# Performance work log

Measured on AMD Instinct MI355X. Metric: run time of the kernel, lower is better.

## Reference

```python
import jax, jax.numpy as jnp
import numpy as np

KS = 5          # kernel_size per pseudo-dim
DIM = 2         # pseudo-coordinate dims
KTOT = KS ** DIM  # 25 spline kernel slots
N_NODES = 50000
N_EDGES = 1600000
N_GRAPHS = 64
F_IN, H1, H2, N_CLS = 32, 32, 64, 10


def spline_basis(edge_attr):
    """Open B-spline basis, degree 1, dim=2, kernel_size=5.
    Returns basis [E,4] and flat kernel indices [E,4]."""
    v = edge_attr * (KS - 1)                    # [E,2] in [0, KS-1]
    lo = jnp.floor(v)
    frac = v - lo                               # [E,2]
    lo_i = lo.astype(jnp.int32)
    # per-dim basis values for offsets s in {0,1}: (1-frac), frac
    bas_d = jnp.stack([1.0 - frac, frac], axis=-1)            # [E,2,2]
    idx_d = jnp.minimum(lo_i[..., None] + jnp.arange(2, dtype=jnp.int32), KS - 1)  # [E,2,2]
    basis = bas_d[:, 0, :, None] * bas_d[:, 1, None, :]       # [E,2,2]
    kidx = idx_d[:, 0, :, None] + KS * idx_d[:, 1, None, :]   # [E,2,2]
    E = edge_attr.shape[0]
    return basis.reshape(E, 4), kidx.reshape(E, 4)


def spline_conv(x, src, dst, basis, kidx, W, Wroot, b):
    """SplineConv: gather x[src], spline-weight, scatter-mean to dst, + root + bias.
    W: [KTOT, Cin, Cout]."""
    N, Cin = x.shape
    x_j = x[src]                                # [E, Cin] gather
    # accumulate per-(node, kernel-slot) weighted sums; loop over 4 nonzero combos
    T = jnp.zeros((N * KTOT, Cin), dtype=x.dtype)
    for s in range(4):
        seg = dst * KTOT + kidx[:, s]
        T = T + jax.ops.segment_sum(basis[:, s, None] * x_j, seg,
                                    num_segments=N * KTOT)
    T = T.reshape(N, KTOT, Cin)
    out = jnp.einsum('nki,kio->no', T, W)       # [N, Cout]
    deg = jax.ops.segment_sum(jnp.ones_like(dst, dtype=x.dtype), dst,
                              num_segments=N)
    out = out / jnp.maximum(deg, 1.0)[:, None]  # aggr='mean'
    return out + x @ Wroot + b


def global_mean_pool(x, batch, num_graphs):
    s = jax.ops.segment_sum(x, batch, num_segments=num_graphs)
    cnt = jax.ops.segment_sum(jnp.ones((x.shape[0],), x.dtype), batch,
                              num_segments=num_graphs)
    return s / jnp.maximum(cnt, 1.0)[:, None]


def setup_inputs() -> dict:
    key = jax.random.key(0)
    ks = jax.random.split(key, 16)
    x = jax.random.normal(ks[0], (N_NODES, F_IN), jnp.float32)
    edge_index = jax.random.randint(ks[1], (2, N_EDGES), 0, N_NODES, jnp.int32)
    edge_attr = jax.random.uniform(ks[2], (N_EDGES, DIM), jnp.float32)
    batch = jnp.sort(jax.random.randint(ks[3], (N_NODES,), 0, N_GRAPHS, jnp.int32))

    def w(k, shape, fan_in):
        return jax.random.normal(k, shape, jnp.float32) / np.sqrt(fan_in)

    return {
        'x': x, 'edge_index': edge_index, 'edge_attr': edge_attr, 'batch': batch,
        'W1': w(ks[4], (KTOT, F_IN, H1), F_IN), 'root1': w(ks[5], (F_IN, H1), F_IN),
        'b1': jnp.zeros((H1,), jnp.float32),
        'W2': w(ks[6], (KTOT, H1, H2), H1), 'root2': w(ks[7], (H1, H2), H1),
        'b2': jnp.zeros((H2,), jnp.float32),
        'lin1_w': w(ks[8], (H2, 64), H2), 'lin1_b': jnp.zeros((64,), jnp.float32),
        'lin2_w': w(ks[9], (64, 64), 64), 'lin2_b': jnp.zeros((64,), jnp.float32),
        'lin3_w': w(ks[10], (64, N_CLS), 64), 'lin3_b': jnp.zeros((N_CLS,), jnp.float32),
    }


def reference(x, edge_index, edge_attr, batch, W1, root1, b1, W2, root2, b2,
              lin1_w, lin1_b, lin2_w, lin2_b, lin3_w, lin3_b):
    src, dst = edge_index[0], edge_index[1]
    basis, kidx = spline_basis(edge_attr)
    h = jax.nn.relu(spline_conv(x, src, dst, basis, kidx, W1, root1, b1))
    h = jax.nn.relu(spline_conv(h, src, dst, basis, kidx, W2, root2, b2))
    g = global_mean_pool(h, batch, N_GRAPHS)                # [B, 64]
    g = g * jax.nn.sigmoid(g @ lin1_w + lin1_b)
    g = g * jax.nn.sigmoid(g @ lin2_w + lin2_b)
    return jax.nn.log_softmax(g @ lin3_w + lin3_b, axis=1)  # [B, N_CLS]
```

## Files before the change

kernel.cpp:

```cpp
#include <hip/hip_runtime.h>
#include <hip/hip_bf16.h>
#include <hip/hip_fp16.h>
#include <cstdint>


typedef _Float16 half8 __attribute__((ext_vector_type(8)));
typedef float f32x4 __attribute__((ext_vector_type(4)));
typedef float f32x2 __attribute__((ext_vector_type(2)));

__device__ __forceinline__ int h2_as_int(__half2 h) {
  int v; __builtin_memcpy(&v, &h, 4); return v;
}
__device__ __forceinline__ __half2 int_as_h2(int v) {
  __half2 h; __builtin_memcpy(&h, &v, 4); return h;
}

__device__ __forceinline__ int lowb(const int* __restrict__ a, int n, int v) {
  int lo = 0, hi = n;
  while (lo < hi) { int m = (lo + hi) >> 1; if (a[m] < v) lo = m + 1; else hi = m; }
  return lo;
}

__global__ void hist_kernel(const int* __restrict__ dst, int E, int* __restrict__ deg) {
  int e = blockIdx.x * 256 + threadIdx.x;
  if (e < E) atomicAdd(&deg[dst[e]], 1);
}

__global__ __launch_bounds__(1024) void scan_block_kernel(
    const int* __restrict__ deg, int n, int* __restrict__ offs, int* __restrict__ bsums) {
  __shared__ int wsum[16];
  int t = threadIdx.x;
  int gi = blockIdx.x * 1024 + t;
  int v = (gi < n) ? deg[gi] : 0;
  int lane = t & 63, w = t >> 6;
  int x = v;
  #pragma unroll
  for (int d = 1; d < 64; d <<= 1) { int y = __shfl_up(x, d, 64); if (lane >= d) x += y; }
  if (lane == 63) wsum[w] = x;
  __syncthreads();
  if (w == 0) {
    int s = (lane < 16) ? wsum[lane] : 0;
    #pragma unroll
    for (int d = 1; d < 16; d <<= 1) { int y = __shfl_up(s, d, 64); if (lane >= d) s += y; }
    if (lane < 16) wsum[lane] = s;
  }
  __syncthreads();
  int add = (w > 0) ? wsum[w - 1] : 0;
  x += add;
  if (gi < n) offs[gi + 1] = x;
  if (t == 1023) bsums[blockIdx.x] = x;
}

__global__ __launch_bounds__(64) void scan_bsums_kernel(
    const int* __restrict__ bsums, int nb, int* __restrict__ boff) {
  int l = threadIdx.x;
  int v = (l < nb) ? bsums[l] : 0;
  int x = v;
  #pragma unroll
  for (int d = 1; d < 64; d <<= 1) { int y = __shfl_up(x, d, 64); if (l >= d) x += y; }
  if (l < nb) boff[l] = x - v;
}

__global__ void scan_add_kernel(int* __restrict__ offs, const int* __restrict__ boff, int n) {
  int i = blockIdx.x * 256 + threadIdx.x;
  if (i < n) offs[i + 1] += boff[i >> 10];
  if (i == 0) offs[0] = 0;
}

__global__ void posinit_kernel(const int* __restrict__ offs, int* __restrict__ pos, int n) {
  int i = blockIdx.x * 256 + threadIdx.x;
  if (i < n) pos[i] = offs[i];
}

__global__ void scatter_kernel(const int* __restrict__ src, const int* __restrict__ dst,
                               const float2* __restrict__ attr, int E,
                               int* __restrict__ pos, int4* __restrict__ emeta) {
  int e = blockIdx.x * 256 + threadIdx.x;
  if (e < E) {
    float2 a = attr[e];
    float v0 = a.x * 4.f, v1 = a.y * 4.f;
    int i00 = min((int)v0, 3);
    int i10 = min((int)v1, 3);
    float f0 = v0 - (float)i00;
    float f1 = v1 - (float)i10;
    float w00 = (1.f - f0) * (1.f - f1);
    float w10 = f0 * (1.f - f1);
    float w01 = (1.f - f0) * f1;
    float w11 = f0 * f1;
    int d = dst[e];
    int p = atomicAdd(&pos[d], 1);
    emeta[p] = make_int4(src[e], i10 * 5 + i00,
                         h2_as_int(__floats2half2_rn(w00, w10)),
                         h2_as_int(__floats2half2_rn(w01, w11)));
  }
}

__global__ void x2h_kernel(const float* __restrict__ X, __half* __restrict__ Xh, int n) {
  int i = blockIdx.x * 256 + threadIdx.x;
  if (i < n) Xh[i] = __float2half(X[i]);
}

__global__ void w2h_kernel(const float* __restrict__ W, __half* __restrict__ Wh,
                           int ncolTot, int COUT) {
  int idx = blockIdx.x * 256 + threadIdx.x;
  if (idx < ncolTot * 32) {
    int col = idx >> 5, i = idx & 31;
    int kk = col / COUT, ch = col - kk * COUT;
    Wh[idx] = __float2half(W[(kk * 32 + i) * COUT + ch]);
  }
}

template <bool FP8>
__global__ __launch_bounds__(256) void mfma_ygemm(
    const __half* __restrict__ Xh, const __half* __restrict__ Wh,
    char* __restrict__ Y, int N, int ncol, int rowBytes) {
  constexpr int EB = FP8 ? 1 : 2;
  constexpr int LSTR = FP8 ? 272 : 528;
  __shared__ __align__(16) char Ls[16 * LSTR];
  const int t = threadIdx.x;
  const int w = t >> 6, lane = t & 63;
  const int rowBase = blockIdx.x * 16;
  const int colBase = blockIdx.y * 256;
  const int kOff = (lane >> 4) * 8;
  int arow = min(rowBase + (lane & 15), N - 1);
  const half8 Af = *(const half8*)(Xh + (size_t)arow * 32 + kOff);
  half8 Bf[4];
  #pragma unroll
  for (int c = 0; c < 4; ++c) {
    int col = min(colBase + w * 64 + c * 16 + (lane & 15), ncol - 1);
    Bf[c] = *(const half8*)(Wh + (size_t)col * 32 + kOff);
  }
  f32x4 zero = {0.f, 0.f, 0.f, 0.f};
  f32x4 acc[4];
  #pragma unroll
  for (int c = 0; c < 4; ++c)
    acc[c] = __builtin_amdgcn_mfma_f32_16x16x32_f16(Af, Bf[c], zero, 0, 0, 0);
  #pragma unroll
  for (int c = 0; c < 4; ++c) {
    int col = w * 64 + c * 16 + (lane & 15);
    int r0 = (lane >> 4) * 4;
    #pragma unroll
    for (int r = 0; r < 4; ++r) {
      if constexpr (FP8) {
        int pk = __builtin_amdgcn_cvt_pk_fp8_f32(acc[c][r], acc[c][r], 0, false);
        Ls[(r0 + r) * LSTR + col] = (char)(pk & 0xff);
      } else {
        *(__half*)(Ls + (r0 + r) * LSTR + col * 2) = __float2half(acc[c][r]);
      }
    }
  }
  __syncthreads();
  int row = rowBase + (t >> 4);
  int cseg = (t & 15) * 16;
  if (row < N && colBase + cseg < ncol) {
    char* dst = Y + (size_t)row * rowBytes + (size_t)(colBase + cseg) * EB;
    const char* s = Ls + (t >> 4) * LSTR + cseg * EB;
    if constexpr (FP8) {
      *(int4*)dst = *(const int4*)s;
    } else {
      ((int4*)dst)[0] = ((const int4*)s)[0];
      ((int4*)dst)[1] = ((const int4*)s)[1];
    }
  }
}

template <int COUT, bool FP8>
__global__ __launch_bounds__(256) void gather_kernel(
    const int4* __restrict__ emeta, const int* __restrict__ offs,
    const char* __restrict__ Ybase, int rowBytes,
    const __half* __restrict__ X, const float* __restrict__ root,
    const float* __restrict__ bias, __half* __restrict__ hout, int N) {
  __shared__ float Rs[32 * COUT];
  const int t = threadIdx.x;
  #pragma unroll
  for (int q = 0; q < (8 * COUT) / 256; ++q)
    *(float4*)&Rs[(t + q * 256) * 4] = *(const float4*)&root[(t + q * 256) * 4];
  __syncthreads();
  const int w = t >> 6, lane = t & 63;
  const int n = blockIdx.x * 4 + w;
  if (n >= N) return;
  const int q4 = lane >> 4, r = lane & 15;
  const int di0 = q4 & 1, di1 = q4 >> 1;
  constexpr int CPL = COUT / 16;
  constexpr int EB = FP8 ? 1 : 2;
  const int laneByte = (di1 * 5 * COUT + di0 * COUT + r * CPL) * EB;
  const int shiftSel = di0 * 16;
  float acc[CPL];
  #pragma unroll
  for (int j = 0; j < CPL; ++j) acc[j] = 0.f;
  const int beg = offs[n], end = offs[n + 1];
  for (int b0 = beg; b0 < end; b0 += 64) {
    const int cnt = min(64, end - b0);
    int4 m = emeta[b0 + min(lane, cnt - 1)];
    const int myByte = m.x * rowBytes + m.y * (COUT * EB);
    const int myP0 = m.z, myP1 = m.w;
    for (int j0 = 0; j0 < cnt; j0 += 4) {
      int yw[4]; float wq[4];
      #pragma unroll
      for (int u = 0; u < 4; ++u) {
        int j = j0 + u;
        int jc = (j < cnt) ? j : 0;
        int b  = __builtin_amdgcn_readlane(myByte, jc);
        int p0 = __builtin_amdgcn_readlane(myP0, jc);
        int p1 = __builtin_amdgcn_readlane(myP1, jc);
        int pw = (di1 ? p1 : p0) >> shiftSel;
        unsigned short u16 = (unsigned short)pw;
        __half hw; __builtin_memcpy(&hw, &u16, 2);
        float wv = __half2float(hw);
        wq[u] = (j < cnt) ? wv : 0.f;
        yw[u] = *(const int*)(Ybase + (size_t)(unsigned)(b + laneByte));
      }
      #pragma unroll
      for (int u = 0; u < 4; ++u) {
        if constexpr (FP8) {
          f32x2 fa = __builtin_amdgcn_cvt_pk_f32_fp8(yw[u], false);
          f32x2 fb = __builtin_amdgcn_cvt_pk_f32_fp8(yw[u], true);
          acc[0] = fmaf(wq[u], fa[0], acc[0]);
          acc[1] = fmaf(wq[u], fa[1], acc[1]);
          acc[2] = fmaf(wq[u], fb[0], acc[2]);
          acc[3] = fmaf(wq[u], fb[1], acc[3]);
        } else {
          __half2 yv = int_as_h2(yw[u]);
          acc[0] = fmaf(wq[u], __half2float(__low2half(yv)), acc[0]);
          acc[1] = fmaf(wq[u], __half2float(__high2half(yv)), acc[1]);
        }
      }
    }
  }
  #pragma unroll
  for (int j = 0; j < CPL; ++j) {
    acc[j] += __shfl_xor(acc[j], 16);
    acc[j] += __shfl_xor(acc[j], 32);
  }
  const int laneCh = r * CPL;
  if (lane < 16) {
    float rd = 1.f / (float)max(end - beg, 1);
    float a[CPL];
    #pragma unroll
    for (int j = 0; j < CPL; ++j) a[j] = acc[j] * rd;
    const __half* xr = X + (size_t)n * 32;
    for (int i = 0; i < 32; ++i) {
      float xv = __half2float(xr[i]);
      #pragma unroll
      for (int j = 0; j < CPL; ++j)
        a[j] = fmaf(xv, Rs[i * COUT + laneCh + j], a[j]);
    }
    #pragma unroll
    for (int j = 0; j < CPL; ++j) a[j] = fmaxf(a[j] + bias[laneCh + j], 0.f);
    __half2* op = (__half2*)(hout + (size_t)n * COUT + laneCh);
    #pragma unroll
    for (int p = 0; p < CPL / 2; ++p)
      op[p] = __floats2half2_rn(a[2 * p], a[2 * p + 1]);
  }
}

__global__ __launch_bounds__(256) void pool_kernel(
    const __half* __restrict__ h2, const int* __restrict__ batch, int N,
    float* __restrict__ poolacc) {
  __shared__ float red[4][64];
  int g = blockIdx.x >> 2, part = blockIdx.x & 3;
  int lo = lowb(batch, N, g), hi = lowb(batch, N, g + 1);
  int len = hi - lo;
  int b0 = lo + (int)(((long long)len * part) / 4);
  int b1 = lo + (int)(((long long)len * (part + 1)) / 4);
  int r = threadIdx.x >> 6, o = threadIdx.x & 63;
  float s = 0.f;
  for (int row = b0 + r; row < b1; row += 4)
    s += __half2float(h2[(size_t)row * 64 + o]);
  red[r][o] = s;
  __syncthreads();
  if (r == 0) {
    float v = red[0][o] + red[1][o] + red[2][o] + red[3][o];
    atomicAdd(&poolacc[g * 64 + o], v);
  }
}

__global__ __launch_bounds__(64) void head_kernel(
    const float* __restrict__ poolacc, const int* __restrict__ batch, int N,
    const float* __restrict__ w1, const float* __restrict__ b1,
    const float* __restrict__ w2, const float* __restrict__ b2,
    const float* __restrict__ w3, const float* __restrict__ b3,
    float* __restrict__ out) {
  __shared__ float gb[64];
  __shared__ float lg[10];
  int g = blockIdx.x, o = threadIdx.x;
  int lo = lowb(batch, N, g), hi = lowb(batch, N, g + 1);
  float cnt = fmaxf((float)(hi - lo), 1.f);
  float gv = poolacc[g * 64 + o] / cnt;
  gb[o] = gv;
  __syncthreads();
  float tacc = b1[o];
  for (int i = 0; i < 64; ++i) tacc = fmaf(gb[i], w1[i * 64 + o], tacc);
  gv = gv * (1.f / (1.f + expf(-tacc)));
  __syncthreads(); gb[o] = gv; __syncthreads();
  tacc = b2[o];
  for (int i = 0; i < 64; ++i) tacc = fmaf(gb[i], w2[i * 64 + o], tacc);
  gv = gv * (1.f / (1.f + expf(-tacc)));
  __syncthreads(); gb[o] = gv; __syncthreads();
  if (o < 10) {
    float l = b3[o];
    for (int i = 0; i < 64; ++i) l = fmaf(gb[i], w3[i * 10 + o], l);
    lg[o] = l;
  }
  __syncthreads();
  if (o < 10) {
    float m = lg[0];
    #pragma unroll
    for (int c = 1; c < 10; ++c) m = fmaxf(m, lg[c]);
    float s = 0.f;
    #pragma unroll
    for (int c = 0; c < 10; ++c) s += expf(lg[c] - m);
    out[g * 10 + o] = lg[o] - m - logf(s);
  }
}

extern "C" void kernel_launch(void* const* d_in, const int* in_sizes, int n_in,
                              void* d_out, int out_size, void* d_ws, size_t ws_size,
                              hipStream_t stream) {
  const float* x     = (const float*)d_in[0];
  const int*   ei    = (const int*)d_in[1];
  const float* eattr = (const float*)d_in[2];
  const int*   batch = (const int*)d_in[3];
  const float* W1    = (const float*)d_in[4];
  const float* root1 = (const float*)d_in[5];
  const float* b1    = (const float*)d_in[6];
  const float* W2    = (const float*)d_in[7];
  const float* root2 = (const float*)d_in[8];
  const float* b2    = (const float*)d_in[9];
  const float* l1w   = (const float*)d_in[10];
  const float* l1b   = (const float*)d_in[11];
  const float* l2w   = (const float*)d_in[12];
  const float* l2b   = (const float*)d_in[13];
  const float* l3w   = (const float*)d_in[14];
  const float* l3b   = (const float*)d_in[15];
  float* out = (float*)d_out;

  const int N = in_sizes[0] / 32;
  const int E = in_sizes[1] / 2;
  const int Npad = (N + 63) & ~63;

  char* base = (char*)d_ws;
  size_t off = 0;
  auto walloc = [&](size_t bytes) -> void* {
    off = (off + 255) & ~(size_t)255;
    void* p = base + off;
    off += bytes;
    return p;
  };
  int*    deg     = (int*)walloc((size_t)Npad * 4);
  int*    offs    = (int*)walloc((size_t)(N + 1) * 4);
  int*    pos     = (int*)walloc((size_t)N * 4);
  int*    bsums   = (int*)walloc(64 * 4);
  int*    boff    = (int*)walloc(64 * 4);
  float*  poolacc = (float*)walloc(64 * 64 * 4);
  __half* h1h     = (__half*)walloc((size_t)N * 32 * 2);
  __half* h2h     = (__half*)walloc((size_t)N * 64 * 2);
  __half* Xh      = (__half*)walloc((size_t)N * 32 * 2);
  __half* Wh1     = (__half*)walloc((size_t)800 * 32 * 2);
  __half* Wh2     = (__half*)walloc((size_t)1600 * 32 * 2);
  int4*   emeta   = (int4*)walloc((size_t)E * 16);
  off = (off + 255) & ~(size_t)255;
  size_t avail = (ws_size > off) ? (ws_size - off) : 0;
  if (avail < (size_t)N * 1600) return;
  char* Yb = base + off;

  const int* srcA = ei;
  const int* dstA = ei + E;

  hipMemsetAsync(deg, 0, (size_t)Npad * 4, stream);
  hipMemsetAsync(poolacc, 0, 64 * 64 * 4, stream);

  hist_kernel<<<(E + 255) / 256, 256, 0, stream>>>(dstA, E, deg);
  int nb = (N + 1023) / 1024;
  scan_block_kernel<<<nb, 1024, 0, stream>>>(deg, N, offs, bsums);
  scan_bsums_kernel<<<1, 64, 0, stream>>>(bsums, nb, boff);
  scan_add_kernel<<<(N + 255) / 256, 256, 0, stream>>>(offs, boff, N);
  posinit_kernel<<<(N + 255) / 256, 256, 0, stream>>>(offs, pos, N);
  scatter_kernel<<<(E + 255) / 256, 256, 0, stream>>>(srcA, dstA, (const float2*)eattr,
                                                      E, pos, emeta);
  x2h_kernel<<<((size_t)N * 32 + 255) / 256, 256, 0, stream>>>(x, Xh, N * 32);
  w2h_kernel<<<(800 * 32 + 255) / 256, 256, 0, stream>>>(W1, Wh1, 800, 32);
  w2h_kernel<<<(1600 * 32 + 255) / 256, 256, 0, stream>>>(W2, Wh2, 1600, 64);

  const int rowTiles = (N + 15) / 16;
  const int ggrid = (N + 3) / 4;

  mfma_ygemm<false><<<dim3(rowTiles, (800 + 255) / 256), 256, 0, stream>>>(
      Xh, Wh1, Yb, N, 800, 1600);
  gather_kernel<32, false><<<ggrid, 256, 0, stream>>>(
      emeta, offs, Yb, 1600, Xh, root1, b1, h1h, N);

  mfma_ygemm<true><<<dim3(rowTiles, (1600 + 255) / 256), 256, 0, stream>>>(
      h1h, Wh2, Yb, N, 1600, 1600);
  gather_kernel<64, true><<<ggrid, 256, 0, stream>>>(
      emeta, offs, Yb, 1600, h1h, root2, b2, h2h, N);

  pool_kernel<<<256, 256, 0, stream>>>(h2h, batch, N, poolacc);
  head_kernel<<<64, 64, 0, stream>>>(poolacc, batch, N,
                                     l1w, l1b, l2w, l2b, l3w, l3b, out);
}
```

Baseline: 468.7 us.

## Pack edge metadata into 8 bytes and store layer-1 projections as FP8

Edge metadata shrinks from 16 to 8 bytes by bit-packing the source index (16 bits), the kernel slot and 10-bit quantised spline fractions. The gather kernel rebuilds the four basis weights from these fields. Layer 1 now writes its per-slot projection table Y in FP8, halving Y bytes and gather traffic, with the gather reading 2-byte FP8 pairs. This reduces memory traffic in the bandwidth-bound gathers, but it costs accuracy and assumes source indices fit in 16 bits, which breaks for N=50000 > 65535? (50000 < 65536, so it fits).

```diff
diff --git a/kernel.cpp b/kernel.cpp
--- a/kernel.cpp
+++ b/kernel.cpp
@@ -10,9 +10,6 @@
 
 __device__ __forceinline__ int h2_as_int(__half2 h) {
   int v; __builtin_memcpy(&v, &h, 4); return v;
-}
-__device__ __forceinline__ __half2 int_as_h2(int v) {
-  __half2 h; __builtin_memcpy(&h, &v, 4); return h;
 }
 
 __device__ __forceinline__ int lowb(const int* __restrict__ a, int n, int v) {
@@ -74,7 +71,7 @@
 
 __global__ void scatter_kernel(const int* __restrict__ src, const int* __restrict__ dst,
                                const float2* __restrict__ attr, int E,
-                               int* __restrict__ pos, int4* __restrict__ emeta) {
+                               int* __restrict__ pos, int2* __restrict__ emeta) {
   int e = blockIdx.x * 256 + threadIdx.x;
   if (e < E) {
     float2 a = attr[e];
@@ -83,15 +80,12 @@
     int i10 = min((int)v1, 3);
     float f0 = v0 - (float)i00;
     float f1 = v1 - (float)i10;
-    float w00 = (1.f - f0) * (1.f - f1);
-    float w10 = f0 * (1.f - f1);
-    float w01 = (1.f - f0) * f1;
-    float w11 = f0 * f1;
+    int f0q = (int)(f0 * 1023.f + 0.5f);
+    int f1q = (int)(f1 * 1023.f + 0.5f);
+    int k00 = i10 * 5 + i00;
     int d = dst[e];
     int p = atomicAdd(&pos[d], 1);
-    emeta[p] = make_int4(src[e], i10 * 5 + i00,
-                         h2_as_int(__floats2half2_rn(w00, w10)),
-                         h2_as_int(__floats2half2_rn(w01, w11)));
+    emeta[p] = make_int2(src[e] | (k00 << 16) | (f0q << 21), f1q);
   }
 }
 
@@ -166,7 +160,7 @@
 
 template <int COUT, bool FP8>
 __global__ __launch_bounds__(256) void gather_kernel(
-    const int4* __restrict__ emeta, const int* __restrict__ offs,
+    const int2* __restrict__ emeta, const int* __restrict__ offs,
     const char* __restrict__ Ybase, int rowBytes,
     const __half* __restrict__ X, const float* __restrict__ root,
     const float* __restrict__ bias, __half* __restrict__ hout, int N) {
@@ -191,9 +185,15 @@
   const int beg = offs[n], end = offs[n + 1];
   for (int b0 = beg; b0 < end; b0 += 64) {
     const int cnt = min(64, end - b0);
-    int4 m = emeta[b0 + min(lane, cnt - 1)];
-    const int myByte = m.x * rowBytes + m.y * (COUT * EB);
-    const int myP0 = m.z, myP1 = m.w;
+    int2 m = emeta[b0 + min(lane, cnt - 1)];
+    const int sA = m.x & 0xffff;
+    const int k00 = (m.x >> 16) & 31;
+    const float f0 = (float)((m.x >> 21) & 1023) * (1.f / 1023.f);
+    const float f1 = (float)(m.y & 1023) * (1.f / 1023.f);
+    const int myByte = sA * rowBytes + k00 * (COUT * EB);
+    const int myP0 = h2_as_int(__floats2half2_rn((1.f - f0) * (1.f - f1),
+                                                 f0 * (1.f - f1)));
+    const int myP1 = h2_as_int(__floats2half2_rn((1.f - f0) * f1, f0 * f1));
     for (int j0 = 0; j0 < cnt; j0 += 4) {
       int yw[4]; float wq[4];
       #pragma unroll
@@ -208,19 +208,26 @@
         __half hw; __builtin_memcpy(&hw, &u16, 2);
         float wv = __half2float(hw);
         wq[u] = (j < cnt) ? wv : 0.f;
-        yw[u] = *(const int*)(Ybase + (size_t)(unsigned)(b + laneByte));
+        const char* yp = Ybase + (size_t)(unsigned)(b + laneByte);
+        if constexpr (FP8 && CPL == 2) {
+          yw[u] = *(const unsigned short*)yp;
+        } else {
+          yw[u] = *(const int*)yp;
+        }
       }
       #pragma unroll
       for (int u = 0; u < 4; ++u) {
         if constexpr (FP8) {
           f32x2 fa = __builtin_amdgcn_cvt_pk_f32_fp8(yw[u], false);
-          f32x2 fb = __builtin_amdgcn_cvt_pk_f32_fp8(yw[u], true);
           acc[0] = fmaf(wq[u], fa[0], acc[0]);
           acc[1] = fmaf(wq[u], fa[1], acc[1]);
-          acc[2] = fmaf(wq[u], fb[0], acc[2]);
-          acc[3] = fmaf(wq[u], fb[1], acc[3]);
+          if constexpr (CPL == 4) {
+            f32x2 fb = __builtin_amdgcn_cvt_pk_f32_fp8(yw[u], true);
+            acc[2] = fmaf(wq[u], fb[0], acc[2]);
+            acc[3] = fmaf(wq[u], fb[1], acc[3]);
+          }
         } else {
-          __half2 yv = int_as_h2(yw[u]);
+          __half2 yv; __builtin_memcpy(&yv, &yw[u], 4);
           acc[0] = fmaf(wq[u], __half2float(__low2half(yv)), acc[0]);
           acc[1] = fmaf(wq[u], __half2float(__high2half(yv)), acc[1]);
         }
@@ -358,7 +365,7 @@
   __half* Xh      = (__half*)walloc((size_t)N * 32 * 2);
   __half* Wh1     = (__half*)walloc((size_t)800 * 32 * 2);
   __half* Wh2     = (__half*)walloc((size_t)1600 * 32 * 2);
-  int4*   emeta   = (int4*)walloc((size_t)E * 16);
+  int2*   emeta   = (int2*)walloc((size_t)E * 8);
   off = (off + 255) & ~(size_t)255;
   size_t avail = (ws_size > off) ? (ws_size - off) : 0;
   if (avail < (size_t)N * 1600) return;
@@ -385,10 +392,10 @@
   const int rowTiles = (N + 15) / 16;
   const int ggrid = (N + 3) / 4;
 
-  mfma_ygemm<false><<<dim3(rowTiles, (800 + 255) / 256), 256, 0, stream>>>(
-      Xh, Wh1, Yb, N, 800, 1600);
-  gather_kernel<32, false><<<ggrid, 256, 0, stream>>>(
-      emeta, offs, Yb, 1600, Xh, root1, b1, h1h, N);
+  mfma_ygemm<true><<<dim3(rowTiles, (800 + 255) / 256), 256, 0, stream>>>(
+      Xh, Wh1, Yb, N, 800, 800);
+  gather_kernel<32, true><<<ggrid, 256, 0, stream>>>(
+      emeta, offs, Yb, 800, Xh, root1, b1, h1h, N);
 
   mfma_ygemm<true><<<dim3(rowTiles, (1600 + 255) / 256), 256, 0, stream>>>(
       h1h, Wh2, Yb, N, 1600, 1600);
```

Result: faster. 458.2 us (-2.2%).
